# Performance work log

Hardware: AMD Instinct MI355X
Metric: run time of the kernel (lower is better)

Reference implementation:

```python
import jax, jax.numpy as jnp
import numpy as np
import math

B, N, D, H = 1, 128, 256, 8
DK = D // H

def setup_inputs() -> dict:
    key = jax.random.key(0)
    ks = jax.random.split(key, 8)
    query = jax.random.normal(ks[0], (B, N, N, D), dtype=jnp.float32)
    key_t = jax.random.normal(ks[1], (B, N, N, D), dtype=jnp.float32)
    value = jax.random.normal(ks[2], (B, N, N, D), dtype=jnp.float32)
    mask = jax.random.randint(ks[3], (B, N, N, N), 0, 2).astype(jnp.bool_)
    s = 1.0 / math.sqrt(D)
    # torch nn.Linear weights: [out_features, in_features]
    Wk = jax.random.uniform(ks[4], (D, D), dtype=jnp.float32, minval=-s, maxval=s)
    Wv = jax.random.uniform(ks[5], (D, D), dtype=jnp.float32, minval=-s, maxval=s)
    Wq = jax.random.uniform(ks[6], (D, D), dtype=jnp.float32, minval=-s, maxval=s)
    Wo = jax.random.uniform(ks[7], (D, D), dtype=jnp.float32, minval=-s, maxval=s)
    return {"query": query, "key": key_t, "value": value, "mask": mask,
            "Wq": Wq, "Wk": Wk, "Wv": Wv, "Wo": Wo}

def reference(query, key, value, mask, Wq, Wk, Wv, Wo):
    b, n = query.shape[0], query.shape[1]
    # linear projections (no bias), then split heads -> [b, n, n, h, d_k]
    q = (query @ Wq.T).reshape(b, n, n, H, DK)
    k = (key @ Wk.T).reshape(b, n, n, H, DK)
    v = (value @ Wv.T).reshape(b, n, n, H, DK)
    scale = 1.0 / math.sqrt(DK)
    neg = jnp.float32(-1e9)
    m = mask[..., None]  # [b, n, n, n, 1] broadcast over heads
    # row attention: edge (x,y) attends over edges (x,z)
    scores_r = jnp.einsum('bxyhd,bxzhd->bxyzh', q, k) * scale
    scores_r = jnp.where(m, neg, scores_r)
    # column attention: edge (x,y) attends over edges (z,y)
    scores_l = jnp.einsum('bxyhd,bzyhd->bxyzh', q, k) * scale
    scores_l = jnp.where(m, neg, scores_l)
    scores = jnp.concatenate((scores_r, scores_l), axis=3)  # [b,n,n,2n,h]
    att = jax.nn.softmax(scores, axis=3)
    att_r, att_l = att[:, :, :, :n], att[:, :, :, n:]
    x_r = jnp.einsum('bxyzh,bxzhd->bxyhd', att_r, v)
    x_l = jnp.einsum('bxyzh,bzyhd->bxyhd', att_l, v)
    x = (x_r + x_l).reshape(b, n, n, D)
    return x @ Wo.T
```

## Files before the change

### kernel.cpp

```cpp
#include <hip/hip_runtime.h>
#include <hip/hip_bf16.h>
#include <math.h>

#define N_DIM 128
#define NH 8
#define DKH 32
#define M_ROWS (N_DIM * N_DIM)

typedef __attribute__((ext_vector_type(8))) short bf16x8;
typedef __attribute__((ext_vector_type(4))) float f32x4;

__device__ inline ushort f2b(float x) {
    union { __hip_bfloat16 b; ushort u; } c;
    c.b = __float2bfloat16(x);
    return c.u;
}

#define GLDS(src, dst) \
    __builtin_amdgcn_global_load_lds((const __attribute__((address_space(1))) void*)(src), \
                                     (__attribute__((address_space(3))) void*)(dst), 16, 0, 0)

__global__ __launch_bounds__(256) void cvt_w_kernel(const float* __restrict__ w0,
                                                    const float* __restrict__ w1,
                                                    const float* __restrict__ w2,
                                                    const float* __restrict__ w3,
                                                    ushort* __restrict__ out) {
    const int b = blockIdx.x;
    const int m = b >> 6;
    const float* src = (m == 0) ? w0 : (m == 1) ? w1 : (m == 2) ? w2 : w3;
    const int off = (b & 63) * 1024 + threadIdx.x * 4;
    float4 v = *(const float4*)(src + off);
    union { ushort u[4]; short4 s4; } p;
    p.u[0] = f2b(v.x); p.u[1] = f2b(v.y); p.u[2] = f2b(v.z); p.u[3] = f2b(v.w);
    *(short4*)(out + (size_t)m * 65536 + off) = p.s4;
}

__global__ __launch_bounds__(256) void pack_mask(const int* __restrict__ mask,
                                                 ulonglong2* __restrict__ P,
                                                 ulonglong2* __restrict__ PT) {
    const int row = blockIdx.x * 4 + (threadIdx.x >> 6);
    const int lane = threadIdx.x & 63;
    const int* mrow = mask + (size_t)row * 128;
    unsigned long long lo = __ballot(mrow[lane] != 0);
    unsigned long long hi = __ballot(mrow[64 + lane] != 0);
    if (lane == 0) {
        ulonglong2 v; v.x = lo; v.y = hi;
        P[row] = v;
        PT[(row & 127) * 128 + (row >> 7)] = v;
    }
}

template <bool AF32, bool OBF16, bool BATCHED>
__global__ __launch_bounds__(512) void gemm2(const void* __restrict__ A0,
                                             const void* __restrict__ A1,
                                             const void* __restrict__ A2,
                                             const ushort* __restrict__ Wbase,
                                             void* __restrict__ Cbase,
                                             float oscale0) {
    __shared__ ushort As[2][32 * 64];
    __shared__ ushort Ws[2][256 * 64];
    const int tid = threadIdx.x;
    const int w = tid >> 6, l = tid & 63;
    const int lr = l & 15, g = l >> 4;
    const int row0 = blockIdx.x * 32;

    const void* Ain = A0;
    const ushort* W = Wbase;
    float oscale = oscale0;
    size_t coff = 0;
    if (BATCHED) {
        const int y = blockIdx.y;
        Ain = (y == 0) ? A0 : (y == 1) ? A1 : A2;
        W += (size_t)y * 65536;
        coff = (size_t)y * (M_ROWS * 256);
        oscale = (y == 0) ? oscale0 : 1.0f;
    }

    const int lrow = l >> 3;
    const int kof = ((l & 7) ^ lrow) * 8;

    auto stage = [&](int t, int buf) {
        const int kbase = t * 64;
#pragma unroll
        for (int i = 0; i < 4; i++) {
            const int chunk = i * 8 + w;
            GLDS(W + (size_t)(chunk * 8 + lrow) * 256 + kbase + kof,
                 &Ws[buf][chunk * 512]);
        }
        if (AF32) {
            const float* Af = (const float*)Ain;
            const int r = tid >> 4, k0 = (tid & 15) * 4;
            float4 v = *(const float4*)(Af + (size_t)(row0 + r) * 256 + kbase + k0);
            union { ushort u[4]; short4 s4; } p;
            p.u[0] = f2b(v.x); p.u[1] = f2b(v.y); p.u[2] = f2b(v.z); p.u[3] = f2b(v.w);
            int byte = (r * 128 + k0 * 2) ^ ((r & 7) << 4);
            *(short4*)((char*)&As[buf][0] + byte) = p.s4;
        } else {
            if (w < 4) {
                const ushort* Ab = (const ushort*)Ain;
                GLDS(Ab + (size_t)(row0 + w * 8 + lrow) * 256 + kbase + kof,
                     &As[buf][w * 512]);
            }
        }
    };

    f32x4 acc[2][2];
    const f32x4 zero = {0.f, 0.f, 0.f, 0.f};
    acc[0][0] = zero; acc[0][1] = zero; acc[1][0] = zero; acc[1][1] = zero;

    stage(0, 0);
    __syncthreads();

#pragma unroll
    for (int t = 0; t < 4; t++) {
        const int cur = t & 1;
        if (t < 3) stage(t + 1, cur ^ 1);
#pragma unroll
        for (int kk = 0; kk < 2; kk++) {
            bf16x8 a[2], b[2];
#pragma unroll
            for (int fr = 0; fr < 2; fr++) {
                const int r = fr * 16 + lr;
                int byte = r * 128 + kk * 64 + g * 16;
                byte ^= (r & 7) << 4;
                a[fr] = *(const bf16x8*)((const char*)&As[cur][0] + byte);
            }
#pragma unroll
            for (int fc = 0; fc < 2; fc++) {
                const int r = w * 32 + fc * 16 + lr;
                int byte = r * 128 + kk * 64 + g * 16;
                byte ^= (r & 7) << 4;
                b[fc] = *(const bf16x8*)((const char*)&Ws[cur][0] + byte);
            }
#pragma unroll
            for (int fr = 0; fr < 2; fr++)
#pragma unroll
                for (int fc = 0; fc < 2; fc++)
                    acc[fr][fc] = __builtin_amdgcn_mfma_f32_16x16x32_bf16(a[fr], b[fc], acc[fr][fc], 0, 0, 0);
        }
        __syncthreads();
    }

#pragma unroll
    for (int fr = 0; fr < 2; fr++)
#pragma unroll
        for (int fc = 0; fc < 2; fc++)
#pragma unroll
            for (int j = 0; j < 4; j++) {
                const int row = row0 + fr * 16 + g * 4 + j;
                const int col = w * 32 + fc * 16 + lr;
                const float vv = acc[fr][fc][j] * oscale;
                if (OBF16) ((ushort*)Cbase)[coff + (size_t)row * 256 + col] = f2b(vv);
                else       ((float*)Cbase)[(size_t)row * 256 + col] = vv;
            }
}

template <int PASS>
__global__ __launch_bounds__(256) void attn_pass(const ushort* __restrict__ qb,
                                                 const ushort* __restrict__ kb,
                                                 const ushort* __restrict__ vb,
                                                 const ulonglong2* __restrict__ Pm,
                                                 float* __restrict__ ml,
                                                 float* __restrict__ sl,
                                                 float* __restrict__ Pl,
                                                 ushort* __restrict__ xb) {
    __shared__ ushort Qs[128 * 40];
    __shared__ ushort Ks[128 * 40];
    __shared__ ushort Vt[32 * 128];
    __shared__ ushort Ats[128 * 128];
    __shared__ ulonglong2 Ms[128];
    __shared__ float mlq[128], slq[128];

    const int tid = threadIdx.x;
    const int fixed = blockIdx.x >> 3;
    const int h = blockIdx.x & 7;

    int base, stride;
    if (PASS == 0) {
        base = (fixed * NH + h) * DKH;
        stride = N_DIM * NH * DKH;
    } else {
        base = fixed * N_DIM * NH * DKH + h * DKH;
        stride = NH * DKH;
    }

    if (tid < 128) {
        Ms[tid] = Pm[fixed * 128 + tid];
        if (PASS == 1) mlq[tid] = ml[(tid * NH + h) * N_DIM + fixed];
    } else if (PASS == 1) {
        slq[tid - 128] = sl[((tid - 128) * NH + h) * N_DIM + fixed];
    }

#pragma unroll
    for (int i = 0; i < 2; i++) {
        int idx = tid + i * 256;
        int r = idx >> 2, d0 = (idx & 3) * 8;
        size_t goff = (size_t)base + (size_t)r * stride + d0;
        int4 qv = *(const int4*)(qb + goff);
        *(int4*)&Qs[r * 40 + d0] = qv;
        int4 kv = *(const int4*)(kb + goff);
        *(int4*)&Ks[r * 40 + d0] = kv;
        union { int4 v4; ushort u[8]; } uu;
        uu.v4 = *(const int4*)(vb + goff);
#pragma unroll
        for (int j = 0; j < 8; j++) {
            int d = d0 + j;
            int byte = d * 256 + r * 2;
            byte ^= (d & 7) << 4;
            Vt[byte >> 1] = uu.u[j];
        }
    }
    __syncthreads();

    const int w = tid >> 6;
    const int lane = tid & 63;
    const int lr = lane & 15;
    const int g = lane >> 4;
    const int rbase = w * 32;

    bf16x8 aq[2];
#pragma unroll
    for (int fr = 0; fr < 2; fr++)
        aq[fr] = *(const bf16x8*)&Qs[(rbase + fr * 16 + lr) * 40 + g * 8];

    f32x4 s[2][8];
    const f32x4 zero = {0.f, 0.f, 0.f, 0.f};
#pragma unroll
    for (int fc = 0; fc < 8; fc++) {
        bf16x8 bk = *(const bf16x8*)&Ks[(fc * 16 + lr) * 40 + g * 8];
#pragma unroll
        for (int fr = 0; fr < 2; fr++)
            s[fr][fc] = __builtin_amdgcn_mfma_f32_16x16x32_bf16(aq[fr], bk, zero, 0, 0, 0);
    }

    float mx[2][4], sm[2][4];
#pragma unroll
    for (int fr = 0; fr < 2; fr++) {
#pragma unroll
        for (int j = 0; j < 4; j++) {
            const int row = rbase + fr * 16 + g * 4 + j;
            const ulonglong2 mb = Ms[row];
            const unsigned long long mls = mb.x >> lr;
            const unsigned long long mhs = mb.y >> lr;
            float mmax = -3.0e38f;
#pragma unroll
            for (int fc = 0; fc < 8; fc++) {
                const int bit = (int)(((fc < 4 ? mls : mhs) >> ((fc & 3) * 16)) & 1ull);
                float val = bit ? -1.0e9f : s[fr][fc][j];
                s[fr][fc][j] = val;
                mmax = fmaxf(mmax, val);
            }
            mmax = fmaxf(mmax, __shfl_xor(mmax, 1));
            mmax = fmaxf(mmax, __shfl_xor(mmax, 2));
            mmax = fmaxf(mmax, __shfl_xor(mmax, 4));
            mmax = fmaxf(mmax, __shfl_xor(mmax, 8));
            float ssum = 0.f;
#pragma unroll
            for (int fc = 0; fc < 8; fc++) {
                const int col = fc * 16 + lr;
                float e = __expf(s[fr][fc][j] - mmax);
                ssum += e;
                int byte = row * 256 + col * 2;
                byte ^= (row & 7) << 4;
                Ats[byte >> 1] = f2b(e);
            }
            ssum += __shfl_xor(ssum, 1);
            ssum += __shfl_xor(ssum, 2);
            ssum += __shfl_xor(ssum, 4);
            ssum += __shfl_xor(ssum, 8);
            mx[fr][j] = mmax;
            sm[fr][j] = ssum;
        }
    }
    __syncthreads();

    f32x4 p[2][2];
    p[0][0] = zero; p[0][1] = zero; p[1][0] = zero; p[1][1] = zero;
#pragma unroll
    for (int ks = 0; ks < 4; ks++) {
        bf16x8 pa[2];
#pragma unroll
        for (int fr = 0; fr < 2; fr++) {
            const int row = rbase + fr * 16 + lr;
            int byte = row * 256 + ks * 64 + g * 16;
            byte ^= (row & 7) << 4;
            pa[fr] = *(const bf16x8*)&Ats[byte >> 1];
        }
#pragma unroll
        for (int fc = 0; fc < 2; fc++) {
            const int rd = fc * 16 + lr;
            int byte = rd * 256 + ks * 64 + g * 16;
            byte ^= (rd & 7) << 4;
            bf16x8 vbf = *(const bf16x8*)&Vt[byte >> 1];
#pragma unroll
            for (int fr = 0; fr < 2; fr++)
                p[fr][fc] = __builtin_amdgcn_mfma_f32_16x16x32_bf16(pa[fr], vbf, p[fr][fc], 0, 0, 0);
        }
    }

    if (PASS == 0) {
#pragma unroll
        for (int fr = 0; fr < 2; fr++) {
#pragma unroll
            for (int j = 0; j < 4; j++) {
                const int row = rbase + fr * 16 + g * 4 + j;
                if (lr == 0) {
                    ml[(fixed * NH + h) * N_DIM + row] = mx[fr][j];
                    sl[(fixed * NH + h) * N_DIM + row] = sm[fr][j];
                }
#pragma unroll
                for (int fc = 0; fc < 2; fc++) {
                    const int d = fc * 16 + lr;
                    Pl[((size_t)(fixed * NH + h) * N_DIM + row) * DKH + d] = p[fr][fc][j];
                }
            }
        }
    } else {
#pragma unroll
        for (int fr = 0; fr < 2; fr++) {
#pragma unroll
            for (int j = 0; j < 4; j++) {
                const int row = rbase + fr * 16 + g * 4 + j;
                const float mr = mx[fr][j], sr = sm[fr][j];
                const float mlv = mlq[row], slv = slq[row];
                const float m = fmaxf(mr, mlv);
                const float cr = __expf(mr - m), cl = __expf(mlv - m);
                const float inv = 1.0f / (sr * cr + slv * cl);
#pragma unroll
                for (int fc = 0; fc < 2; fc++) {
                    const int d = fc * 16 + lr;
                    const float plv = Pl[((size_t)(row * NH + h) * N_DIM + fixed) * DKH + d];
                    const float o = (p[fr][fc][j] * cr + plv * cl) * inv;
                    xb[((size_t)fixed * N_DIM + row) * 256 + h * DKH + d] = f2b(o);
                }
            }
        }
    }
}

extern "C" void kernel_launch(void* const* d_in, const int* in_sizes, int n_in,
                              void* d_out, int out_size, void* d_ws, size_t ws_size,
                              hipStream_t stream) {
    const float* query = (const float*)d_in[0];
    const float* key_t = (const float*)d_in[1];
    const float* value = (const float*)d_in[2];
    const int*   mask  = (const int*)d_in[3];
    const float* Wq    = (const float*)d_in[4];
    const float* Wk    = (const float*)d_in[5];
    const float* Wv    = (const float*)d_in[6];
    const float* Wo    = (const float*)d_in[7];

    const size_t MB = 1024 * 1024;
    char* ws = (char*)d_ws;
    ushort*     qb = (ushort*)ws;
    ushort*     kb = qb + (size_t)M_ROWS * 256;
    ushort*     vb = kb + (size_t)M_ROWS * 256;
    ushort*     xb = (ushort*)(ws + 24 * MB);
    float*      Pl = (float*)(ws + 32 * MB);
    float*      ml = (float*)(ws + 48 * MB);
    float*      sl = (float*)(ws + 48 * MB + 512 * 1024);
    ushort*     Wb = (ushort*)(ws + 49 * MB);
    ulonglong2* Pp = (ulonglong2*)(ws + 50 * MB);
    ulonglong2* PT = (ulonglong2*)(ws + 50 * MB + 256 * 1024);

    const float qscale = 0.17677669529663687f;

    cvt_w_kernel<<<256, 256, 0, stream>>>(Wq, Wk, Wv, Wo, Wb);
    pack_mask<<<4096, 256, 0, stream>>>(mask, Pp, PT);
    gemm2<true, true, true><<<dim3(M_ROWS / 32, 3), 512, 0, stream>>>(
        query, key_t, value, Wb, qb, qscale);
    attn_pass<0><<<N_DIM * NH, 256, 0, stream>>>(qb, kb, vb, PT, ml, sl, Pl, xb);
    attn_pass<1><<<N_DIM * NH, 256, 0, stream>>>(qb, kb, vb, Pp, ml, sl, Pl, xb);
    gemm2<false, false, false><<<dim3(M_ROWS / 32, 1), 512, 0, stream>>>(
        xb, nullptr, nullptr, Wb + 3 * 65536, d_out, 1.0f);
}
```

Measured before the change: 169.3 us.

## Merge prep kernels, load Q fragments directly, transpose Pl layout for coalesced reads

```diff
diff --git a/kernel.cpp b/kernel.cpp
--- a/kernel.cpp
+++ b/kernel.cpp
@@ -20,33 +20,34 @@
     __builtin_amdgcn_global_load_lds((const __attribute__((address_space(1))) void*)(src), \
                                      (__attribute__((address_space(3))) void*)(dst), 16, 0, 0)
 
-__global__ __launch_bounds__(256) void cvt_w_kernel(const float* __restrict__ w0,
-                                                    const float* __restrict__ w1,
-                                                    const float* __restrict__ w2,
-                                                    const float* __restrict__ w3,
-                                                    ushort* __restrict__ out) {
-    const int b = blockIdx.x;
-    const int m = b >> 6;
-    const float* src = (m == 0) ? w0 : (m == 1) ? w1 : (m == 2) ? w2 : w3;
-    const int off = (b & 63) * 1024 + threadIdx.x * 4;
-    float4 v = *(const float4*)(src + off);
-    union { ushort u[4]; short4 s4; } p;
-    p.u[0] = f2b(v.x); p.u[1] = f2b(v.y); p.u[2] = f2b(v.z); p.u[3] = f2b(v.w);
-    *(short4*)(out + (size_t)m * 65536 + off) = p.s4;
-}
-
-__global__ __launch_bounds__(256) void pack_mask(const int* __restrict__ mask,
-                                                 ulonglong2* __restrict__ P,
-                                                 ulonglong2* __restrict__ PT) {
-    const int row = blockIdx.x * 4 + (threadIdx.x >> 6);
-    const int lane = threadIdx.x & 63;
-    const int* mrow = mask + (size_t)row * 128;
-    unsigned long long lo = __ballot(mrow[lane] != 0);
-    unsigned long long hi = __ballot(mrow[64 + lane] != 0);
-    if (lane == 0) {
-        ulonglong2 v; v.x = lo; v.y = hi;
-        P[row] = v;
-        PT[(row & 127) * 128 + (row >> 7)] = v;
+__global__ __launch_bounds__(256) void prep_kernel(const int* __restrict__ mask,
+                                                   ulonglong2* __restrict__ P,
+                                                   ulonglong2* __restrict__ PT,
+                                                   const float* __restrict__ w0,
+                                                   const float* __restrict__ w1,
+                                                   const float* __restrict__ w2,
+                                                   const float* __restrict__ w3,
+                                                   ushort* __restrict__ wout) {
+    if (blockIdx.x < 4096) {
+        const int row = blockIdx.x * 4 + (threadIdx.x >> 6);
+        const int lane = threadIdx.x & 63;
+        const int* mrow = mask + (size_t)row * 128;
+        unsigned long long lo = __ballot(mrow[lane] != 0);
+        unsigned long long hi = __ballot(mrow[64 + lane] != 0);
+        if (lane == 0) {
+            ulonglong2 v; v.x = lo; v.y = hi;
+            P[row] = v;
+            PT[(row & 127) * 128 + (row >> 7)] = v;
+        }
+    } else {
+        const int b = blockIdx.x - 4096;
+        const int m = b >> 6;
+        const float* src = (m == 0) ? w0 : (m == 1) ? w1 : (m == 2) ? w2 : w3;
+        const int off = (b & 63) * 1024 + threadIdx.x * 4;
+        float4 v = *(const float4*)(src + off);
+        union { ushort u[4]; short4 s4; } p;
+        p.u[0] = f2b(v.x); p.u[1] = f2b(v.y); p.u[2] = f2b(v.z); p.u[3] = f2b(v.w);
+        *(short4*)(wout + (size_t)m * 65536 + off) = p.s4;
     }
 }
 
@@ -164,7 +165,6 @@
                                                  float* __restrict__ sl,
                                                  float* __restrict__ Pl,
                                                  ushort* __restrict__ xb) {
-    __shared__ ushort Qs[128 * 40];
     __shared__ ushort Ks[128 * 40];
     __shared__ ushort Vt[32 * 128];
     __shared__ ushort Ats[128 * 128];
@@ -184,20 +184,45 @@
         stride = NH * DKH;
     }
 
+    const int w = tid >> 6;
+    const int lane = tid & 63;
+    const int lr = lane & 15;
+    const int g = lane >> 4;
+    const int rbase = w * 32;
+
     if (tid < 128) {
         Ms[tid] = Pm[fixed * 128 + tid];
-        if (PASS == 1) mlq[tid] = ml[(tid * NH + h) * N_DIM + fixed];
+        if (PASS == 1) mlq[tid] = ml[(fixed * NH + h) * N_DIM + tid];
     } else if (PASS == 1) {
-        slq[tid - 128] = sl[((tid - 128) * NH + h) * N_DIM + fixed];
-    }
+        slq[tid - 128] = sl[(fixed * NH + h) * N_DIM + (tid - 128)];
+    }
+
+    float plv[2][2][4];
+    if (PASS == 1) {
+#pragma unroll
+        for (int fr = 0; fr < 2; fr++)
+#pragma unroll
+            for (int j = 0; j < 4; j++) {
+                const int row = rbase + fr * 16 + g * 4 + j;
+#pragma unroll
+                for (int fc = 0; fc < 2; fc++) {
+                    const int d = fc * 16 + lr;
+                    plv[fr][fc][j] = Pl[((size_t)(fixed * NH + h) * N_DIM + row) * DKH + d];
+                }
+            }
+    }
+
+    bf16x8 aq[2];
+#pragma unroll
+    for (int fr = 0; fr < 2; fr++)
+        aq[fr] = *(const bf16x8*)(qb + (size_t)base +
+                                  (size_t)(rbase + fr * 16 + lr) * stride + g * 8);
 
 #pragma unroll
     for (int i = 0; i < 2; i++) {
         int idx = tid + i * 256;
         int r = idx >> 2, d0 = (idx & 3) * 8;
         size_t goff = (size_t)base + (size_t)r * stride + d0;
-        int4 qv = *(const int4*)(qb + goff);
-        *(int4*)&Qs[r * 40 + d0] = qv;
         int4 kv = *(const int4*)(kb + goff);
         *(int4*)&Ks[r * 40 + d0] = kv;
         union { int4 v4; ushort u[8]; } uu;
@@ -211,17 +236,6 @@
         }
     }
     __syncthreads();
-
-    const int w = tid >> 6;
-    const int lane = tid & 63;
-    const int lr = lane & 15;
-    const int g = lane >> 4;
-    const int rbase = w * 32;
-
-    bf16x8 aq[2];
-#pragma unroll
-    for (int fr = 0; fr < 2; fr++)
-        aq[fr] = *(const bf16x8*)&Qs[(rbase + fr * 16 + lr) * 40 + g * 8];
 
     f32x4 s[2][8];
     const f32x4 zero = {0.f, 0.f, 0.f, 0.f};
@@ -305,13 +319,13 @@
             for (int j = 0; j < 4; j++) {
                 const int row = rbase + fr * 16 + g * 4 + j;
                 if (lr == 0) {
-                    ml[(fixed * NH + h) * N_DIM + row] = mx[fr][j];
-                    sl[(fixed * NH + h) * N_DIM + row] = sm[fr][j];
+                    ml[((size_t)row * NH + h) * N_DIM + fixed] = mx[fr][j];
+                    sl[((size_t)row * NH + h) * N_DIM + fixed] = sm[fr][j];
                 }
 #pragma unroll
                 for (int fc = 0; fc < 2; fc++) {
                     const int d = fc * 16 + lr;
-                    Pl[((size_t)(fixed * NH + h) * N_DIM + row) * DKH + d] = p[fr][fc][j];
+                    Pl[((size_t)(row * NH + h) * N_DIM + fixed) * DKH + d] = p[fr][fc][j];
                 }
             }
         }
@@ -329,8 +343,7 @@
 #pragma unroll
                 for (int fc = 0; fc < 2; fc++) {
                     const int d = fc * 16 + lr;
-                    const float plv = Pl[((size_t)(row * NH + h) * N_DIM + fixed) * DKH + d];
-                    const float o = (p[fr][fc][j] * cr + plv * cl) * inv;
+                    const float o = (p[fr][fc][j] * cr + plv[fr][fc][j] * cl) * inv;
                     xb[((size_t)fixed * N_DIM + row) * 256 + h * DKH + d] = f2b(o);
                 }
             }
@@ -365,8 +378,7 @@
 
     const float qscale = 0.17677669529663687f;
 
-    cvt_w_kernel<<<256, 256, 0, stream>>>(Wq, Wk, Wv, Wo, Wb);
-    pack_mask<<<4096, 256, 0, stream>>>(mask, Pp, PT);
+    prep_kernel<<<4352, 256, 0, stream>>>(mask, Pp, PT, Wq, Wk, Wv, Wo, Wb);
     gemm2<true, true, true><<<dim3(M_ROWS / 32, 3), 512, 0, stream>>>(
         query, key_t, value, Wb, qb, qscale);
     attn_pass<0><<<N_DIM * NH, 256, 0, stream>>>(qb, kb, vb, PT, ml, sl, Pl, xb);
```

New measurement: 167.0 us. About the same (-1.3%).
